# Performance work log

Measured on AMD Instinct MI355X. Metric: run time of the kernel, lower is better.

Reference implementation:

```python
import jax, jax.numpy as jnp
import numpy as np

NEG_SLOPE = 0.2
EPS = 1e-16
HEADS1, OUT1 = 4, 32
HEADS2, OUT2 = 1, 32


def _gat_conv(x, W, a_src, a_dst, bias, src, dst, num_nodes, heads, out_c, concat):
    # x: [N, F_in], W: [F_in, heads*out_c], a_*: [heads, out_c]
    h = (x @ W).reshape(num_nodes, heads, out_c)            # [N, H, C]
    alpha_src = (h * a_src).sum(-1)                          # [N, H]
    alpha_dst = (h * a_dst).sum(-1)                          # [N, H]
    e = jax.nn.leaky_relu(alpha_src[src] + alpha_dst[dst], NEG_SLOPE)  # [E, H]
    # softmax over incoming edges of each destination node (PyG softmax)
    m = jax.ops.segment_max(e, dst, num_segments=num_nodes)
    ex = jnp.exp(e - m[dst])
    s = jax.ops.segment_sum(ex, dst, num_segments=num_nodes)
    alpha = ex / (s[dst] + EPS)                              # [E, H]
    out = jax.ops.segment_sum(h[src] * alpha[:, :, None], dst,
                              num_segments=num_nodes)        # [N, H, C]
    out = out.reshape(num_nodes, heads * out_c) if concat else out.mean(axis=1)
    return out + bias


def setup_inputs() -> dict:
    key = jax.random.key(0)
    ks = jax.random.split(key, 10)
    N, E, F_IN = 50000, 1600000, 128
    sc = 0.1
    return {
        "x": jax.random.normal(ks[0], (N, F_IN), jnp.float32),
        "edge_index": jax.random.randint(ks[1], (2, E), 0, N, jnp.int32),
        "W1": jax.random.normal(ks[2], (F_IN, HEADS1 * OUT1), jnp.float32) * sc,
        "a_src1": jax.random.normal(ks[3], (HEADS1, OUT1), jnp.float32) * sc,
        "a_dst1": jax.random.normal(ks[4], (HEADS1, OUT1), jnp.float32) * sc,
        "b1": jax.random.normal(ks[5], (HEADS1 * OUT1,), jnp.float32) * sc,
        "W2": jax.random.normal(ks[6], (HEADS1 * OUT1, HEADS2 * OUT2), jnp.float32) * sc,
        "a_src2": jax.random.normal(ks[7], (HEADS2, OUT2), jnp.float32) * sc,
        "a_dst2": jax.random.normal(ks[8], (HEADS2, OUT2), jnp.float32) * sc,
        "b2": jax.random.normal(ks[9], (OUT2,), jnp.float32) * sc,
    }


def reference(x, edge_index, W1, a_src1, a_dst1, b1, W2, a_src2, a_dst2, b2):
    N = x.shape[0]
    # PyG GATConv default add_self_loops=True
    loops = jnp.arange(N, dtype=edge_index.dtype)
    src = jnp.concatenate([edge_index[0], loops])
    dst = jnp.concatenate([edge_index[1], loops])
    h = _gat_conv(x, W1, a_src1, a_dst1, b1, src, dst, N, HEADS1, OUT1, True)
    h = jax.nn.elu(h)
    return _gat_conv(h, W2, a_src2, a_dst2, b2, src, dst, N, HEADS2, OUT2, False)
```

## Files before the change

kernel.cpp:

```cpp
#include <hip/hip_runtime.h>
#include <math.h>

#define NEG_SLOPE 0.2f
#define EPSV 1e-16f
#define NPART 8

typedef _Float16 half4 __attribute__((ext_vector_type(4)));
typedef _Float16 half8 __attribute__((ext_vector_type(8)));
typedef float floatx2 __attribute__((ext_vector_type(2)));
typedef float f32x4 __attribute__((ext_vector_type(4)));


__global__ void k_scan_blk(const int* __restrict__ degp, int N,
                           int* __restrict__ rowptr, int* __restrict__ bsum){
    int b = blockIdx.x, t = threadIdx.x;
    int base = b * 1024 + t * 4;
    int v[4];
    #pragma unroll
    for (int j = 0; j < 4; j++){
        int n = base + j, s = 0;
        if (n < N){
            #pragma unroll
            for (int p = 0; p < NPART; p++) s += degp[p * N + n];
        }
        v[j] = s;
    }
    int s = v[0] + v[1] + v[2] + v[3];
    int lane = t & 63, wid = t >> 6;
    int x = s;
    #pragma unroll
    for (int off = 1; off < 64; off <<= 1){
        int y = __shfl_up(x, off, 64);
        if (lane >= off) x += y;
    }
    __shared__ int ws[4];
    if (lane == 63) ws[wid] = x;
    __syncthreads();
    int woff = 0;
    for (int w = 0; w < wid; w++) woff += ws[w];
    int run = woff + x - s;
    #pragma unroll
    for (int j = 0; j < 4; j++){
        if (base + j < N) rowptr[base + j] = run;
        run += v[j];
    }
    if (t == 255) bsum[b] = woff + x;
}

__global__ void k_finalize(const int* __restrict__ bsum, const int* __restrict__ degp,
                           int N, int ET,
                           int* __restrict__ rowptr, int* __restrict__ poff){
    int b = blockIdx.x, t = threadIdx.x;
    int n = b * 256 + t;
    int chunk = (b * 256) >> 10;
    int off = 0;
    for (int c = 0; c < chunk; c++) off += bsum[c];
    if (n < N){
        int r = rowptr[n] + off;
        rowptr[n] = r;
        int run = r;
        #pragma unroll
        for (int p = 0; p < NPART; p++){
            poff[p * N + n] = run;
            run += degp[p * N + n];
        }
    }
    if (n == 0) rowptr[N] = ET;
}

__launch_bounds__(256)
__global__ void k_scatter2(const int* __restrict__ ei, int E, int ET, int N,
                           const int* __restrict__ poff,
                           const unsigned short* __restrict__ rank,
                           int* __restrict__ csr_src){
    int i = blockIdx.x * 256 + threadIdx.x;
    if (i >= ET) return;
    int s, d;
    if (i < E){ s = ei[i]; d = ei[E + i]; } else { s = i - E; d = s; }
    int pr = rank[i];
    int p = pr >> 13, r = pr & 0x1FFF;
    csr_src[poff[p * N + d] + r] = s;
}


__launch_bounds__(256)
__global__ void k_hist(const int* __restrict__ ei, int E, int ET, int N,
                       unsigned int* __restrict__ degp, unsigned short* __restrict__ rank){
    int t = threadIdx.x;
    int p = __builtin_amdgcn_s_getreg((3 << 11) | 20) & 7;
    int base = blockIdx.x * 1024 + t;
    #pragma unroll
    for (int j = 0; j < 4; j++){
        int i = base + j * 256;
        if (i < ET){
            int d = (i < E) ? ei[E + i] : (i - E);
            unsigned r = __hip_atomic_fetch_add(&degp[(size_t)p * N + d], 1u,
                             __ATOMIC_RELAXED, __HIP_MEMORY_SCOPE_WORKGROUP);
            rank[i] = (unsigned short)((p << 13) | r);
        }
    }
}


__global__ void k_pack(const float* __restrict__ W1, const float* __restrict__ a_src,
                       const float* __restrict__ a_dst,
                       _Float16* __restrict__ W1f, _Float16* __restrict__ Uf){
    int b = blockIdx.x, t = threadIdx.x;
    if (b < 32){
        #pragma unroll
        for (int i = 0; i < 2; i++){
            int idx = t + 256 * i;
            int jj = idx & 7, ln = idx >> 3;
            int kt = b & 3, ct = b >> 2;
            int k = kt * 32 + (ln >> 4) * 8 + jj;
            int col = ct * 16 + (ln & 15);
            W1f[b * 512 + idx] = (_Float16)W1[k * 128 + col];
        }
        return;
    }
    __shared__ float U[128 * 8];
    if (t < 128){
        #pragma unroll
        for (int h = 0; h < 4; h++){
            float s = 0.f, d = 0.f;
            for (int cc = 0; cc < 32; cc++){
                float w = W1[t * 128 + h * 32 + cc];
                s += w * a_src[h * 32 + cc];
                d += w * a_dst[h * 32 + cc];
            }
            U[t * 8 + h]     = s;
            U[t * 8 + h + 4] = d;
        }
    }
    __syncthreads();
    for (int idx = t; idx < 4 * 64 * 8; idx += 256){
        int jj = idx & 7, ln = (idx >> 3) & 63, kt = idx >> 9;
        int k = kt * 32 + (ln >> 4) * 8 + jj;
        int col = ln & 15;
        Uf[idx] = (_Float16)(col < 8 ? U[k * 8 + col] : 0.f);
    }
}


__launch_bounds__(256)
__global__ void k_gemm1(const float* __restrict__ x, const _Float16* __restrict__ W1f,
                        const _Float16* __restrict__ Uf,
                        _Float16* __restrict__ h1h, float* __restrict__ asrc1,
                        float* __restrict__ adst1, int N){
    int t = threadIdx.x;
    int w = t >> 6, lane = t & 63;
    int arow = blockIdx.x * 64 + w * 16 + (lane & 15);
    bool arow_ok = (arow < N);
    const float4* xr = (const float4*)&x[(size_t)(arow_ok ? arow : 0) << 7];
    const half8* Wf = (const half8*)W1f;
    const half8* Uv = (const half8*)Uf;

    f32x4 acc[8];
    #pragma unroll
    for (int c = 0; c < 8; c++) acc[c] = (f32x4)0.f;
    f32x4 accA = (f32x4)0.f;

    #pragma unroll
    for (int kt = 0; kt < 4; kt++){
        half8 af;
        if (arow_ok){
            float4 p0 = xr[kt * 8 + (lane >> 4) * 2];
            float4 p1 = xr[kt * 8 + (lane >> 4) * 2 + 1];
            af[0] = (_Float16)p0.x; af[1] = (_Float16)p0.y;
            af[2] = (_Float16)p0.z; af[3] = (_Float16)p0.w;
            af[4] = (_Float16)p1.x; af[5] = (_Float16)p1.y;
            af[6] = (_Float16)p1.z; af[7] = (_Float16)p1.w;
        } else {
            af[0] = (_Float16)0.f; af[1] = (_Float16)0.f;
            af[2] = (_Float16)0.f; af[3] = (_Float16)0.f;
            af[4] = (_Float16)0.f; af[5] = (_Float16)0.f;
            af[6] = (_Float16)0.f; af[7] = (_Float16)0.f;
        }
        #pragma unroll
        for (int ct = 0; ct < 8; ct++){
            half8 bf = Wf[(ct * 4 + kt) * 64 + lane];
            acc[ct] = __builtin_amdgcn_mfma_f32_16x16x32_f16(af, bf, acc[ct], 0, 0, 0);
        }
        half8 uf = Uv[kt * 64 + lane];
        accA = __builtin_amdgcn_mfma_f32_16x16x32_f16(af, uf, accA, 0, 0, 0);
    }

    int g = lane >> 4, j = lane & 15;
    int rowbase = blockIdx.x * 64 + w * 16 + g * 4;
    #pragma unroll
    for (int r = 0; r < 4; r++){
        int n = rowbase + r;
        if (n >= N) continue;
        _Float16* hrow = &h1h[(size_t)n << 7];
        #pragma unroll
        for (int ct = 0; ct < 8; ct++)
            hrow[ct * 16 + j] = (_Float16)acc[ct][r];
        float av = accA[r];
        if (j < 4)            asrc1[n * 4 + j]       = av;
        else if (j < 8)       adst1[n * 4 + (j - 4)] = av;
    }
}


__launch_bounds__(256)
__global__ void k_agg1(const int* __restrict__ rowptr, const int* __restrict__ csr_src,
                       const float* __restrict__ asrc1, const float* __restrict__ adst1,
                       const _Float16* __restrict__ h1h,
                       const float* __restrict__ b1, float* __restrict__ x2, int N){
    int t = threadIdx.x;
    int lane = t & 63;
    int g = lane >> 4, l = lane & 15, head = l >> 2;
    int n = blockIdx.x * 16 + ((t >> 6) << 2) + g;
    bool valid = (n < N);
    int nn = valid ? n : 0;
    int start = rowptr[nn], end = rowptr[nn + 1];
    float adn = adst1[(nn << 2) + head];
    const char* hb = (const char*)h1h;
    const char* ab = (const char*)asrc1;
    int hoff = l << 4;
    int aoff = head << 2;
    floatx2 r0[4], r1[4], r2[4], r3[4];
    #pragma unroll
    for (int j = 0; j < 4; j++){
        r0[j] = (floatx2)0.f; r1[j] = (floatx2)0.f;
        r2[j] = (floatx2)0.f; r3[j] = (floatx2)0.f;
    }
    float s0a = 0.f, s1a = 0.f, s2a = 0.f, s3a = 0.f;
    int i = start;
    for (; i + 3 < end; i += 4){
        int sa = csr_src[i];
        int sb = csr_src[i + 1];
        int sc = csr_src[i + 2];
        int sd = csr_src[i + 3];
        float ea = *(const float*)(ab + (sa << 4) + aoff) + adn;
        float eb = *(const float*)(ab + (sb << 4) + aoff) + adn;
        float ec = *(const float*)(ab + (sc << 4) + aoff) + adn;
        float ed = *(const float*)(ab + (sd << 4) + aoff) + adn;
        ea = fmaxf(ea, NEG_SLOPE * ea);
        eb = fmaxf(eb, NEG_SLOPE * eb);
        ec = fmaxf(ec, NEG_SLOPE * ec);
        ed = fmaxf(ed, NEG_SLOPE * ed);
        float wa = __expf(ea);
        float wb = __expf(eb);
        float wc = __expf(ec);
        float wd = __expf(ed);
        half8 ha = *(const half8*)(hb + (sa << 8) + hoff);
        half8 hbv = *(const half8*)(hb + (sb << 8) + hoff);
        half8 hcv = *(const half8*)(hb + (sc << 8) + hoff);
        half8 hdv = *(const half8*)(hb + (sd << 8) + hoff);
        s0a += wa; s1a += wb; s2a += wc; s3a += wd;
        floatx2 wa2 = {wa, wa}, wb2 = {wb, wb}, wc2 = {wc, wc}, wd2 = {wd, wd};
        #pragma unroll
        for (int j = 0; j < 4; j++){
            floatx2 ca = {(float)ha[2*j], (float)ha[2*j+1]};
            floatx2 cb = {(float)hbv[2*j], (float)hbv[2*j+1]};
            floatx2 cc = {(float)hcv[2*j], (float)hcv[2*j+1]};
            floatx2 cd = {(float)hdv[2*j], (float)hdv[2*j+1]};
            r0[j] = wa2 * ca + r0[j];
            r1[j] = wb2 * cb + r1[j];
            r2[j] = wc2 * cc + r2[j];
            r3[j] = wd2 * cd + r3[j];
        }
    }
    for (; i < end; i++){
        int sa = csr_src[i];
        float ea = *(const float*)(ab + (sa << 4) + aoff) + adn;
        ea = fmaxf(ea, NEG_SLOPE * ea);
        float wa = __expf(ea);
        half8 ha = *(const half8*)(hb + (sa << 8) + hoff);
        s0a += wa;
        floatx2 wa2 = {wa, wa};
        #pragma unroll
        for (int j = 0; j < 4; j++){
            floatx2 ca = {(float)ha[2*j], (float)ha[2*j+1]};
            r0[j] = wa2 * ca + r0[j];
        }
    }
    if (valid){
        float ssum = (s0a + s1a) + (s2a + s3a);
        float inv = 1.f / (ssum + EPSV);
        float o[8];
        #pragma unroll
        for (int j = 0; j < 4; j++){
            floatx2 c = (r0[j] + r1[j]) + (r2[j] + r3[j]);
            float v0 = c.x * inv + b1[l * 8 + 2*j];
            float v1 = c.y * inv + b1[l * 8 + 2*j + 1];
            o[2*j]   = (v0 > 0.f) ? v0 : expm1f(v0);
            o[2*j+1] = (v1 > 0.f) ? v1 : expm1f(v1);
        }
        float4 o0 = {o[0], o[1], o[2], o[3]};
        float4 o1 = {o[4], o[5], o[6], o[7]};
        *(float4*)&x2[((size_t)n << 7) + (l << 3)]     = o0;
        *(float4*)&x2[((size_t)n << 7) + (l << 3) + 4] = o1;
    }
}


__launch_bounds__(256)
__global__ void k_gemm2(const float* __restrict__ x2, const float* __restrict__ W2,
                        const float* __restrict__ a_src, const float* __restrict__ a_dst,
                        _Float16* __restrict__ h2h, float* __restrict__ asrc2,
                        float* __restrict__ adst2, int N){
    __shared__ float Wl[128 * 32];
    __shared__ float xl[64 * 128];
    int t = threadIdx.x;
    int cg = t & 7, ns = t >> 3;
    for (int idx = t; idx < 1024; idx += 256)
        *(float4*)&Wl[idx * 4] = *(const float4*)&W2[idx * 4];
    int n0 = blockIdx.x * 64;
    for (int idx = t; idx < 2048; idx += 256){
        int row = idx >> 5, k4 = idx & 31;
        float4 v = {0.f, 0.f, 0.f, 0.f};
        if (n0 + row < N) v = *(const float4*)&x2[(size_t)(n0 + row) * 128 + k4 * 4];
        *(float4*)&xl[row * 128 + k4 * 4] = v;
    }
    __syncthreads();
    float4 acc0 = {0,0,0,0}, acc1 = {0,0,0,0};
    #pragma unroll 2
    for (int k = 0; k < 128; k += 4){
        float4 xv0 = *(float4*)&xl[(ns      ) * 128 + k];
        float4 xv1 = *(float4*)&xl[(ns + 32) * 128 + k];
        #pragma unroll
        for (int kk = 0; kk < 4; kk++){
            float4 w = *(float4*)&Wl[(k + kk) * 32 + cg * 4];
            float x0 = ((float*)&xv0)[kk];
            float x1 = ((float*)&xv1)[kk];
            acc0.x = fmaf(x0, w.x, acc0.x); acc0.y = fmaf(x0, w.y, acc0.y);
            acc0.z = fmaf(x0, w.z, acc0.z); acc0.w = fmaf(x0, w.w, acc0.w);
            acc1.x = fmaf(x1, w.x, acc1.x); acc1.y = fmaf(x1, w.y, acc1.y);
            acc1.z = fmaf(x1, w.z, acc1.z); acc1.w = fmaf(x1, w.w, acc1.w);
        }
    }
    float4 a4s = *(const float4*)&a_src[cg * 4];
    float4 a4d = *(const float4*)&a_dst[cg * 4];
    float4 accs[2] = {acc0, acc1};
    #pragma unroll
    for (int j = 0; j < 2; j++){
        int n = n0 + ns + 32 * j;
        if (n >= N) continue;
        float4 a = accs[j];
        half4 hv;
        hv.x = (_Float16)a.x; hv.y = (_Float16)a.y;
        hv.z = (_Float16)a.z; hv.w = (_Float16)a.w;
        *(half4*)&h2h[((size_t)n << 5) + (cg << 2)] = hv;
        float vs = a.x * a4s.x + a.y * a4s.y + a.z * a4s.z + a.w * a4s.w;
        float vd = a.x * a4d.x + a.y * a4d.y + a.z * a4d.z + a.w * a4d.w;
        #pragma unroll
        for (int m = 1; m <= 4; m <<= 1){
            vs += __shfl_xor(vs, m, 64);
            vd += __shfl_xor(vd, m, 64);
        }
        if (cg == 0){ asrc2[n] = vs; adst2[n] = vd; }
    }
}


__launch_bounds__(256)
__global__ void k_agg2(const int* __restrict__ rowptr, const int* __restrict__ csr_src,
                       const float* __restrict__ asrc2, const float* __restrict__ adst2,
                       const _Float16* __restrict__ h2h,
                       const float* __restrict__ b2, float* __restrict__ out, int N){
    int t = threadIdx.x;
    int lane = t & 63;
    int g = lane >> 3, l = lane & 7;
    int n = blockIdx.x * 32 + ((t >> 6) << 3) + g;
    bool valid = (n < N);
    int nn = valid ? n : 0;
    int start = rowptr[nn], end = rowptr[nn + 1];
    float adn = adst2[nn];
    const char* hb = (const char*)h2h;
    const char* ab = (const char*)asrc2;
    int hoff = l << 3;
    floatx2 a0[2], a1[2], a2[2], a3[2];
    a0[0] = (floatx2)0.f; a0[1] = (floatx2)0.f;
    a1[0] = (floatx2)0.f; a1[1] = (floatx2)0.f;
    a2[0] = (floatx2)0.f; a2[1] = (floatx2)0.f;
    a3[0] = (floatx2)0.f; a3[1] = (floatx2)0.f;
    float s0a = 0.f, s1a = 0.f, s2a = 0.f, s3a = 0.f;
    int i = start;
    for (; i + 3 < end; i += 4){
        int sa = csr_src[i];
        int sb = csr_src[i + 1];
        int sc = csr_src[i + 2];
        int sd = csr_src[i + 3];
        float ea = *(const float*)(ab + (sa << 2)) + adn;
        float eb = *(const float*)(ab + (sb << 2)) + adn;
        float ec = *(const float*)(ab + (sc << 2)) + adn;
        float ed = *(const float*)(ab + (sd << 2)) + adn;
        ea = fmaxf(ea, NEG_SLOPE * ea);
        eb = fmaxf(eb, NEG_SLOPE * eb);
        ec = fmaxf(ec, NEG_SLOPE * ec);
        ed = fmaxf(ed, NEG_SLOPE * ed);
        float wa = __expf(ea);
        float wb = __expf(eb);
        float wc = __expf(ec);
        float wd = __expf(ed);
        half4 ha = *(const half4*)(hb + (sa << 6) + hoff);
        half4 hbv = *(const half4*)(hb + (sb << 6) + hoff);
        half4 hcv = *(const half4*)(hb + (sc << 6) + hoff);
        half4 hdv = *(const half4*)(hb + (sd << 6) + hoff);
        s0a += wa; s1a += wb; s2a += wc; s3a += wd;
        floatx2 wa2 = {wa, wa}, wb2 = {wb, wb}, wc2 = {wc, wc}, wd2 = {wd, wd};
        floatx2 ca0 = {(float)ha.x, (float)ha.y},  ca1 = {(float)ha.z, (float)ha.w};
        floatx2 cb0 = {(float)hbv.x, (float)hbv.y}, cb1 = {(float)hbv.z, (float)hbv.w};
        floatx2 cc0 = {(float)hcv.x, (float)hcv.y}, cc1 = {(float)hcv.z, (float)hcv.w};
        floatx2 cd0 = {(float)hdv.x, (float)hdv.y}, cd1 = {(float)hdv.z, (float)hdv.w};
        a0[0] = wa2 * ca0 + a0[0]; a0[1] = wa2 * ca1 + a0[1];
        a1[0] = wb2 * cb0 + a1[0]; a1[1] = wb2 * cb1 + a1[1];
        a2[0] = wc2 * cc0 + a2[0]; a2[1] = wc2 * cc1 + a2[1];
        a3[0] = wd2 * cd0 + a3[0]; a3[1] = wd2 * cd1 + a3[1];
    }
    for (; i < end; i++){
        int sa = csr_src[i];
        float ea = *(const float*)(ab + (sa << 2)) + adn;
        ea = fmaxf(ea, NEG_SLOPE * ea);
        float wa = __expf(ea);
        half4 ha = *(const half4*)(hb + (sa << 6) + hoff);
        s0a += wa;
        floatx2 wa2 = {wa, wa};
        floatx2 ca0 = {(float)ha.x, (float)ha.y}, ca1 = {(float)ha.z, (float)ha.w};
        a0[0] = wa2 * ca0 + a0[0]; a0[1] = wa2 * ca1 + a0[1];
    }
    if (valid){
        floatx2 m0 = (a0[0] + a1[0]) + (a2[0] + a3[0]);
        floatx2 m1 = (a0[1] + a1[1]) + (a2[1] + a3[1]);
        float ssum = (s0a + s1a) + (s2a + s3a);
        float inv = 1.f / (ssum + EPSV);
        const float4 b4 = *(const float4*)&b2[l * 4];
        float4 o;
        o.x = m0.x * inv + b4.x; o.y = m0.y * inv + b4.y;
        o.z = m1.x * inv + b4.z; o.w = m1.y * inv + b4.w;
        *(float4*)&out[((size_t)n << 5) + (l << 2)] = o;
    }
}


extern "C" void kernel_launch(void* const* d_in, const int* in_sizes, int n_in,
                              void* d_out, int out_size, void* d_ws, size_t ws_size,
                              hipStream_t stream){
    const float* x      = (const float*)d_in[0];
    const int*   ei     = (const int*)  d_in[1];
    const float* W1     = (const float*)d_in[2];
    const float* a_src1 = (const float*)d_in[3];
    const float* a_dst1 = (const float*)d_in[4];
    const float* b1     = (const float*)d_in[5];
    const float* W2     = (const float*)d_in[6];
    const float* a_src2 = (const float*)d_in[7];
    const float* a_dst2 = (const float*)d_in[8];
    const float* b2     = (const float*)d_in[9];
    float* out = (float*)d_out;

    int N  = in_sizes[0] / 128;
    int E  = in_sizes[1] / 2;
    int ET = E + N;
    int nScanBlk = (N + 1023) / 1024;
    int G  = (ET + 255) / 256;
    int GH = (ET + 1023) / 1024;
    int nGemmBlk = (N + 63) / 64;

    char* ws = (char*)d_ws;
    size_t off = 0;
    auto alloc = [&](size_t bytes) -> char* {
        char* p = ws + off;
        off += (bytes + 255) & ~(size_t)255;
        return p;
    };
    int*            degp    = (int*)           alloc((size_t)NPART * N * 4);
    int*            rowptr  = (int*)           alloc((size_t)(N + 1) * 4);
    int*            bsum    = (int*)           alloc((size_t)nScanBlk * 4);
    unsigned short* rank    = (unsigned short*)alloc((size_t)ET * 2);
    int*            poff    = (int*)           alloc((size_t)NPART * N * 4);
    int*            csr_src = (int*)           alloc((size_t)ET * 4);
    _Float16*       h1h     = (_Float16*)      alloc((size_t)N * 128 * 2);
    float*          x2      = (float*)         alloc((size_t)N * 128 * 4);
    float*          asrc1   = (float*)         alloc((size_t)N * 4 * 4);
    float*          adst1   = (float*)         alloc((size_t)N * 4 * 4);
    _Float16*       h2h     = (_Float16*)      alloc((size_t)N * 32 * 2);
    float*          asrc2   = (float*)         alloc((size_t)N * 4);
    float*          adst2   = (float*)         alloc((size_t)N * 4);
    _Float16*       W1f     = (_Float16*)      alloc((size_t)32 * 512 * 2);
    _Float16*       Uf      = (_Float16*)      alloc((size_t)4 * 512 * 2);

    hipMemsetAsync(degp, 0, (size_t)NPART * N * 4, stream);
    hipLaunchKernelGGL(k_pack,   dim3(33), dim3(256), 0, stream, W1, a_src1, a_dst1, W1f, Uf);
    hipLaunchKernelGGL(k_hist,   dim3(GH), dim3(256), 0, stream, ei, E, ET, N, (unsigned int*)degp, rank);
    hipLaunchKernelGGL(k_gemm1,  dim3(nGemmBlk), dim3(256), 0, stream, x, W1f, Uf, h1h, asrc1, adst1, N);
    hipLaunchKernelGGL(k_scan_blk,  dim3(nScanBlk), dim3(256), 0, stream, degp, N, rowptr, bsum);
    hipLaunchKernelGGL(k_finalize,  dim3((N + 255) / 256), dim3(256), 0, stream, bsum, degp, N, ET, rowptr, poff);
    hipLaunchKernelGGL(k_scatter2,  dim3(G), dim3(256), 0, stream, ei, E, ET, N, poff, rank, csr_src);
    hipLaunchKernelGGL(k_agg1,      dim3((N + 15) / 16), dim3(256), 0, stream, rowptr, csr_src, asrc1, adst1, h1h, b1, x2, N);
    hipLaunchKernelGGL(k_gemm2,     dim3((N + 63) / 64), dim3(256), 0, stream, x2, W2, a_src2, a_dst2, h2h, asrc2, adst2, N);
    hipLaunchKernelGGL(k_agg2,      dim3((N + 31) / 32), dim3(256), 0, stream, rowptr, csr_src, asrc2, adst2, h2h, b2, out, N);
}
```

Measured before the change: 314.3 us.

## Precompute per-edge attention weights in CSR scatter and unroll layer-1 aggregation by eight

The CSR scatter kernel now also computes the leaky-ReLU and exp attention weight for all four heads of each edge. It writes them to a new per-edge float4 buffer in CSR order. The layer-1 aggregation reads these weights contiguously instead of gathering source attention scores and recomputing exp, and its main loop is unrolled from four to eight edges. This removes per-edge exp work and the random score gathers from aggregation, at the cost of an extra 16-byte scattered write and read per edge.

```diff
diff --git a/kernel.cpp b/kernel.cpp
--- a/kernel.cpp
+++ b/kernel.cpp
@@ -69,17 +69,30 @@
 }
 
 __launch_bounds__(256)
-__global__ void k_scatter2(const int* __restrict__ ei, int E, int ET, int N,
-                           const int* __restrict__ poff,
-                           const unsigned short* __restrict__ rank,
-                           int* __restrict__ csr_src){
+__global__ void k_scatter_w(const int* __restrict__ ei, int E, int ET, int N,
+                            const int* __restrict__ poff,
+                            const unsigned short* __restrict__ rank,
+                            const float* __restrict__ asrc1, const float* __restrict__ adst1,
+                            int* __restrict__ csr_src, float4* __restrict__ w4buf){
     int i = blockIdx.x * 256 + threadIdx.x;
     if (i >= ET) return;
     int s, d;
     if (i < E){ s = ei[i]; d = ei[E + i]; } else { s = i - E; d = s; }
     int pr = rank[i];
     int p = pr >> 13, r = pr & 0x1FFF;
-    csr_src[poff[p * N + d] + r] = s;
+    int pos = poff[p * N + d] + r;
+    csr_src[pos] = s;
+    float4 as = *(const float4*)&asrc1[s << 2];
+    float4 ad = *(const float4*)&adst1[d << 2];
+    float4 e = {as.x + ad.x, as.y + ad.y, as.z + ad.z, as.w + ad.w};
+    e.x = fmaxf(e.x, NEG_SLOPE * e.x);
+    e.y = fmaxf(e.y, NEG_SLOPE * e.y);
+    e.z = fmaxf(e.z, NEG_SLOPE * e.z);
+    e.w = fmaxf(e.w, NEG_SLOPE * e.w);
+    float4 w;
+    w.x = __expf(e.x); w.y = __expf(e.y);
+    w.z = __expf(e.z); w.w = __expf(e.w);
+    w4buf[pos] = w;
 }
 
 
@@ -204,7 +217,7 @@
 
 __launch_bounds__(256)
 __global__ void k_agg1(const int* __restrict__ rowptr, const int* __restrict__ csr_src,
-                       const float* __restrict__ asrc1, const float* __restrict__ adst1,
+                       const float* __restrict__ wbuf4,
                        const _Float16* __restrict__ h1h,
                        const float* __restrict__ b1, float* __restrict__ x2, int N){
     int t = threadIdx.x;
@@ -214,11 +227,10 @@
     bool valid = (n < N);
     int nn = valid ? n : 0;
     int start = rowptr[nn], end = rowptr[nn + 1];
-    float adn = adst1[(nn << 2) + head];
     const char* hb = (const char*)h1h;
-    const char* ab = (const char*)asrc1;
+    const char* wb = (const char*)wbuf4;
     int hoff = l << 4;
-    int aoff = head << 2;
+    int woff = head << 2;
     floatx2 r0[4], r1[4], r2[4], r3[4];
     #pragma unroll
     for (int j = 0; j < 4; j++){
@@ -227,47 +239,58 @@
     }
     float s0a = 0.f, s1a = 0.f, s2a = 0.f, s3a = 0.f;
     int i = start;
-    for (; i + 3 < end; i += 4){
+    for (; i + 7 < end; i += 8){
         int sa = csr_src[i];
         int sb = csr_src[i + 1];
         int sc = csr_src[i + 2];
         int sd = csr_src[i + 3];
-        float ea = *(const float*)(ab + (sa << 4) + aoff) + adn;
-        float eb = *(const float*)(ab + (sb << 4) + aoff) + adn;
-        float ec = *(const float*)(ab + (sc << 4) + aoff) + adn;
-        float ed = *(const float*)(ab + (sd << 4) + aoff) + adn;
-        ea = fmaxf(ea, NEG_SLOPE * ea);
-        eb = fmaxf(eb, NEG_SLOPE * eb);
-        ec = fmaxf(ec, NEG_SLOPE * ec);
-        ed = fmaxf(ed, NEG_SLOPE * ed);
-        float wa = __expf(ea);
-        float wb = __expf(eb);
-        float wc = __expf(ec);
-        float wd = __expf(ed);
-        half8 ha = *(const half8*)(hb + (sa << 8) + hoff);
-        half8 hbv = *(const half8*)(hb + (sb << 8) + hoff);
-        half8 hcv = *(const half8*)(hb + (sc << 8) + hoff);
-        half8 hdv = *(const half8*)(hb + (sd << 8) + hoff);
-        s0a += wa; s1a += wb; s2a += wc; s3a += wd;
-        floatx2 wa2 = {wa, wa}, wb2 = {wb, wb}, wc2 = {wc, wc}, wd2 = {wd, wd};
+        int se = csr_src[i + 4];
+        int sf = csr_src[i + 5];
+        int sg = csr_src[i + 6];
+        int sh = csr_src[i + 7];
+        float wa = *(const float*)(wb + ((size_t)(i    ) << 4) + woff);
+        float wbv= *(const float*)(wb + ((size_t)(i + 1) << 4) + woff);
+        float wc = *(const float*)(wb + ((size_t)(i + 2) << 4) + woff);
+        float wd = *(const float*)(wb + ((size_t)(i + 3) << 4) + woff);
+        float we = *(const float*)(wb + ((size_t)(i + 4) << 4) + woff);
+        float wf = *(const float*)(wb + ((size_t)(i + 5) << 4) + woff);
+        float wg = *(const float*)(wb + ((size_t)(i + 6) << 4) + woff);
+        float wh = *(const float*)(wb + ((size_t)(i + 7) << 4) + woff);
+        half8 ha = *(const half8*)(hb + ((size_t)sa << 8) + hoff);
+        half8 hbx= *(const half8*)(hb + ((size_t)sb << 8) + hoff);
+        half8 hc = *(const half8*)(hb + ((size_t)sc << 8) + hoff);
+        half8 hd = *(const half8*)(hb + ((size_t)sd << 8) + hoff);
+        half8 he = *(const half8*)(hb + ((size_t)se << 8) + hoff);
+        half8 hf = *(const half8*)(hb + ((size_t)sf << 8) + hoff);
+        half8 hg = *(const half8*)(hb + ((size_t)sg << 8) + hoff);
+        half8 hh = *(const half8*)(hb + ((size_t)sh << 8) + hoff);
+        s0a += wa + we; s1a += wbv + wf; s2a += wc + wg; s3a += wd + wh;
+        floatx2 wa2 = {wa, wa}, wb2 = {wbv, wbv}, wc2 = {wc, wc}, wd2 = {wd, wd};
+        floatx2 we2 = {we, we}, wf2 = {wf, wf}, wg2 = {wg, wg}, wh2 = {wh, wh};
         #pragma unroll
         for (int j = 0; j < 4; j++){
-            floatx2 ca = {(float)ha[2*j], (float)ha[2*j+1]};
-            floatx2 cb = {(float)hbv[2*j], (float)hbv[2*j+1]};
-            floatx2 cc = {(float)hcv[2*j], (float)hcv[2*j+1]};
-            floatx2 cd = {(float)hdv[2*j], (float)hdv[2*j+1]};
+            floatx2 ca = {(float)ha[2*j],  (float)ha[2*j+1]};
+            floatx2 cb = {(float)hbx[2*j], (float)hbx[2*j+1]};
+            floatx2 cc = {(float)hc[2*j],  (float)hc[2*j+1]};
+            floatx2 cd = {(float)hd[2*j],  (float)hd[2*j+1]};
+            floatx2 ce = {(float)he[2*j],  (float)he[2*j+1]};
+            floatx2 cf = {(float)hf[2*j],  (float)hf[2*j+1]};
+            floatx2 cg = {(float)hg[2*j],  (float)hg[2*j+1]};
+            floatx2 ch = {(float)hh[2*j],  (float)hh[2*j+1]};
             r0[j] = wa2 * ca + r0[j];
             r1[j] = wb2 * cb + r1[j];
             r2[j] = wc2 * cc + r2[j];
             r3[j] = wd2 * cd + r3[j];
+            r0[j] = we2 * ce + r0[j];
+            r1[j] = wf2 * cf + r1[j];
+            r2[j] = wg2 * cg + r2[j];
+            r3[j] = wh2 * ch + r3[j];
         }
     }
     for (; i < end; i++){
         int sa = csr_src[i];
-        float ea = *(const float*)(ab + (sa << 4) + aoff) + adn;
-        ea = fmaxf(ea, NEG_SLOPE * ea);
-        float wa = __expf(ea);
-        half8 ha = *(const half8*)(hb + (sa << 8) + hoff);
+        float wa = *(const float*)(wb + ((size_t)i << 4) + woff);
+        half8 ha = *(const half8*)(hb + ((size_t)sa << 8) + hoff);
         s0a += wa;
         floatx2 wa2 = {wa, wa};
         #pragma unroll
@@ -480,6 +503,7 @@
     float*          adst2   = (float*)         alloc((size_t)N * 4);
     _Float16*       W1f     = (_Float16*)      alloc((size_t)32 * 512 * 2);
     _Float16*       Uf      = (_Float16*)      alloc((size_t)4 * 512 * 2);
+    float4*         w4buf   = (float4*)        alloc((size_t)ET * 16);
 
     hipMemsetAsync(degp, 0, (size_t)NPART * N * 4, stream);
     hipLaunchKernelGGL(k_pack,   dim3(33), dim3(256), 0, stream, W1, a_src1, a_dst1, W1f, Uf);
@@ -487,8 +511,9 @@
     hipLaunchKernelGGL(k_gemm1,  dim3(nGemmBlk), dim3(256), 0, stream, x, W1f, Uf, h1h, asrc1, adst1, N);
     hipLaunchKernelGGL(k_scan_blk,  dim3(nScanBlk), dim3(256), 0, stream, degp, N, rowptr, bsum);
     hipLaunchKernelGGL(k_finalize,  dim3((N + 255) / 256), dim3(256), 0, stream, bsum, degp, N, ET, rowptr, poff);
-    hipLaunchKernelGGL(k_scatter2,  dim3(G), dim3(256), 0, stream, ei, E, ET, N, poff, rank, csr_src);
-    hipLaunchKernelGGL(k_agg1,      dim3((N + 15) / 16), dim3(256), 0, stream, rowptr, csr_src, asrc1, adst1, h1h, b1, x2, N);
+    hipLaunchKernelGGL(k_scatter_w, dim3(G), dim3(256), 0, stream, ei, E, ET, N, poff, rank,
+                       asrc1, adst1, csr_src, w4buf);
+    hipLaunchKernelGGL(k_agg1,      dim3((N + 15) / 16), dim3(256), 0, stream, rowptr, csr_src, (const float*)w4buf, h1h, b1, x2, N);
     hipLaunchKernelGGL(k_gemm2,     dim3((N + 63) / 64), dim3(256), 0, stream, x2, W2, a_src2, a_dst2, h2h, asrc2, adst2, N);
     hipLaunchKernelGGL(k_agg2,      dim3((N + 31) / 32), dim3(256), 0, stream, rowptr, csr_src, asrc2, adst2, h2h, b2, out, N);
 }
```

New measurement: 349.3 us. 11.1% more time.

## Build CSR with atomic cursors and unroll aggregation gathers by eight

Applied to the files above, without the earlier changes.

Replaces the rank-based CSR build, where the histogram recorded a per-edge rank and the scatter computed positions from it, with a cursor-based scatter. The histogram now only counts degrees, and the scatter claims its slot with an atomicAdd on a per-partition cursor, so the rank array is no longer written or read. The partition is chosen by block index instead of the hardware XCC id, and the atomics move from workgroup scope to device scope. Both aggregation kernels now issue eight neighbour gathers per iteration into scalar FMA accumulators instead of four packed-float2 accumulators, to raise memory-level parallelism. The cost is extra atomic traffic in the scatter, a non-deterministic neighbour order, and higher register pressure in the aggregation kernels.

```diff
diff --git a/kernel.cpp b/kernel.cpp
--- a/kernel.cpp
+++ b/kernel.cpp
@@ -7,7 +7,6 @@
 
 typedef _Float16 half4 __attribute__((ext_vector_type(4)));
 typedef _Float16 half8 __attribute__((ext_vector_type(8)));
-typedef float floatx2 __attribute__((ext_vector_type(2)));
 typedef float f32x4 __attribute__((ext_vector_type(4)));
 
 
@@ -49,7 +48,7 @@
 
 __global__ void k_finalize(const int* __restrict__ bsum, const int* __restrict__ degp,
                            int N, int ET,
-                           int* __restrict__ rowptr, int* __restrict__ poff){
+                           int* __restrict__ rowptr, int* __restrict__ cursor){
     int b = blockIdx.x, t = threadIdx.x;
     int n = b * 256 + t;
     int chunk = (b * 256) >> 10;
@@ -61,44 +60,41 @@
         int run = r;
         #pragma unroll
         for (int p = 0; p < NPART; p++){
-            poff[p * N + n] = run;
+            cursor[p * N + n] = run;
             run += degp[p * N + n];
         }
     }
     if (n == 0) rowptr[N] = ET;
 }
 
-__launch_bounds__(256)
-__global__ void k_scatter2(const int* __restrict__ ei, int E, int ET, int N,
-                           const int* __restrict__ poff,
-                           const unsigned short* __restrict__ rank,
-                           int* __restrict__ csr_src){
+
+__launch_bounds__(256)
+__global__ void k_hist(const int* __restrict__ ei, int E, int ET, int N,
+                       unsigned int* __restrict__ degp){
+    int t = threadIdx.x;
+    int p = blockIdx.x & (NPART - 1);
+    int base = blockIdx.x * 1024 + t;
+    #pragma unroll
+    for (int j = 0; j < 4; j++){
+        int i = base + j * 256;
+        if (i < ET){
+            int d = (i < E) ? ei[E + i] : (i - E);
+            atomicAdd(&degp[(size_t)p * N + d], 1u);
+        }
+    }
+}
+
+
+__launch_bounds__(256)
+__global__ void k_scatter_c(const int* __restrict__ ei, int E, int ET, int N,
+                            int* __restrict__ cursor, int* __restrict__ csr_src){
     int i = blockIdx.x * 256 + threadIdx.x;
     if (i >= ET) return;
     int s, d;
     if (i < E){ s = ei[i]; d = ei[E + i]; } else { s = i - E; d = s; }
-    int pr = rank[i];
-    int p = pr >> 13, r = pr & 0x1FFF;
-    csr_src[poff[p * N + d] + r] = s;
-}
-
-
-__launch_bounds__(256)
-__global__ void k_hist(const int* __restrict__ ei, int E, int ET, int N,
-                       unsigned int* __restrict__ degp, unsigned short* __restrict__ rank){
-    int t = threadIdx.x;
-    int p = __builtin_amdgcn_s_getreg((3 << 11) | 20) & 7;
-    int base = blockIdx.x * 1024 + t;
-    #pragma unroll
-    for (int j = 0; j < 4; j++){
-        int i = base + j * 256;
-        if (i < ET){
-            int d = (i < E) ? ei[E + i] : (i - E);
-            unsigned r = __hip_atomic_fetch_add(&degp[(size_t)p * N + d], 1u,
-                             __ATOMIC_RELAXED, __HIP_MEMORY_SCOPE_WORKGROUP);
-            rank[i] = (unsigned short)((p << 13) | r);
-        }
-    }
+    int p = (i >> 10) & (NPART - 1);
+    int pos = atomicAdd(&cursor[p * N + d], 1);
+    csr_src[pos] = s;
 }
 
 
@@ -219,74 +215,54 @@
     const char* ab = (const char*)asrc1;
     int hoff = l << 4;
     int aoff = head << 2;
-    floatx2 r0[4], r1[4], r2[4], r3[4];
-    #pragma unroll
-    for (int j = 0; j < 4; j++){
-        r0[j] = (floatx2)0.f; r1[j] = (floatx2)0.f;
-        r2[j] = (floatx2)0.f; r3[j] = (floatx2)0.f;
-    }
-    float s0a = 0.f, s1a = 0.f, s2a = 0.f, s3a = 0.f;
+    float acc[8];
+    #pragma unroll
+    for (int j = 0; j < 8; j++) acc[j] = 0.f;
+    float s0 = 0.f, s1 = 0.f, s2 = 0.f, s3 = 0.f;
     int i = start;
-    for (; i + 3 < end; i += 4){
-        int sa = csr_src[i];
-        int sb = csr_src[i + 1];
-        int sc = csr_src[i + 2];
-        int sd = csr_src[i + 3];
-        float ea = *(const float*)(ab + (sa << 4) + aoff) + adn;
-        float eb = *(const float*)(ab + (sb << 4) + aoff) + adn;
-        float ec = *(const float*)(ab + (sc << 4) + aoff) + adn;
-        float ed = *(const float*)(ab + (sd << 4) + aoff) + adn;
-        ea = fmaxf(ea, NEG_SLOPE * ea);
-        eb = fmaxf(eb, NEG_SLOPE * eb);
-        ec = fmaxf(ec, NEG_SLOPE * ec);
-        ed = fmaxf(ed, NEG_SLOPE * ed);
-        float wa = __expf(ea);
-        float wb = __expf(eb);
-        float wc = __expf(ec);
-        float wd = __expf(ed);
-        half8 ha = *(const half8*)(hb + (sa << 8) + hoff);
-        half8 hbv = *(const half8*)(hb + (sb << 8) + hoff);
-        half8 hcv = *(const half8*)(hb + (sc << 8) + hoff);
-        half8 hdv = *(const half8*)(hb + (sd << 8) + hoff);
-        s0a += wa; s1a += wb; s2a += wc; s3a += wd;
-        floatx2 wa2 = {wa, wa}, wb2 = {wb, wb}, wc2 = {wc, wc}, wd2 = {wd, wd};
-        #pragma unroll
-        for (int j = 0; j < 4; j++){
-            floatx2 ca = {(float)ha[2*j], (float)ha[2*j+1]};
-            floatx2 cb = {(float)hbv[2*j], (float)hbv[2*j+1]};
-            floatx2 cc = {(float)hcv[2*j], (float)hcv[2*j+1]};
-            floatx2 cd = {(float)hdv[2*j], (float)hdv[2*j+1]};
-            r0[j] = wa2 * ca + r0[j];
-            r1[j] = wb2 * cb + r1[j];
-            r2[j] = wc2 * cc + r2[j];
-            r3[j] = wd2 * cd + r3[j];
+    for (; i + 7 < end; i += 8){
+        int sv[8];
+        #pragma unroll
+        for (int q = 0; q < 8; q++) sv[q] = csr_src[i + q];
+        half8 hv[8];
+        #pragma unroll
+        for (int q = 0; q < 8; q++)
+            hv[q] = *(const half8*)(hb + ((size_t)sv[q] << 8) + hoff);
+        float wv[8];
+        #pragma unroll
+        for (int q = 0; q < 8; q++){
+            float e = *(const float*)(ab + ((size_t)sv[q] << 4) + aoff) + adn;
+            e = fmaxf(e, NEG_SLOPE * e);
+            wv[q] = __expf(e);
+        }
+        s0 += wv[0] + wv[4]; s1 += wv[1] + wv[5];
+        s2 += wv[2] + wv[6]; s3 += wv[3] + wv[7];
+        #pragma unroll
+        for (int q = 0; q < 8; q++){
+            #pragma unroll
+            for (int j = 0; j < 8; j++)
+                acc[j] = fmaf((float)hv[q][j], wv[q], acc[j]);
         }
     }
     for (; i < end; i++){
         int sa = csr_src[i];
-        float ea = *(const float*)(ab + (sa << 4) + aoff) + adn;
-        ea = fmaxf(ea, NEG_SLOPE * ea);
-        float wa = __expf(ea);
-        half8 ha = *(const half8*)(hb + (sa << 8) + hoff);
-        s0a += wa;
-        floatx2 wa2 = {wa, wa};
-        #pragma unroll
-        for (int j = 0; j < 4; j++){
-            floatx2 ca = {(float)ha[2*j], (float)ha[2*j+1]};
-            r0[j] = wa2 * ca + r0[j];
-        }
+        float e = *(const float*)(ab + ((size_t)sa << 4) + aoff) + adn;
+        e = fmaxf(e, NEG_SLOPE * e);
+        float wa = __expf(e);
+        half8 ha = *(const half8*)(hb + ((size_t)sa << 8) + hoff);
+        s0 += wa;
+        #pragma unroll
+        for (int j = 0; j < 8; j++)
+            acc[j] = fmaf((float)ha[j], wa, acc[j]);
     }
     if (valid){
-        float ssum = (s0a + s1a) + (s2a + s3a);
+        float ssum = (s0 + s1) + (s2 + s3);
         float inv = 1.f / (ssum + EPSV);
         float o[8];
         #pragma unroll
-        for (int j = 0; j < 4; j++){
-            floatx2 c = (r0[j] + r1[j]) + (r2[j] + r3[j]);
-            float v0 = c.x * inv + b1[l * 8 + 2*j];
-            float v1 = c.y * inv + b1[l * 8 + 2*j + 1];
-            o[2*j]   = (v0 > 0.f) ? v0 : expm1f(v0);
-            o[2*j+1] = (v1 > 0.f) ? v1 : expm1f(v1);
+        for (int j = 0; j < 8; j++){
+            float v = acc[j] * inv + b1[l * 8 + j];
+            o[j] = (v > 0.f) ? v : expm1f(v);
         }
         float4 o0 = {o[0], o[1], o[2], o[3]};
         float4 o1 = {o[4], o[5], o[6], o[7]};
@@ -371,65 +347,55 @@
     const char* hb = (const char*)h2h;
     const char* ab = (const char*)asrc2;
     int hoff = l << 3;
-    floatx2 a0[2], a1[2], a2[2], a3[2];
-    a0[0] = (floatx2)0.f; a0[1] = (floatx2)0.f;
-    a1[0] = (floatx2)0.f; a1[1] = (floatx2)0.f;
-    a2[0] = (floatx2)0.f; a2[1] = (floatx2)0.f;
-    a3[0] = (floatx2)0.f; a3[1] = (floatx2)0.f;
-    float s0a = 0.f, s1a = 0.f, s2a = 0.f, s3a = 0.f;
+    float acc[4];
+    #pragma unroll
+    for (int j = 0; j < 4; j++) acc[j] = 0.f;
+    float s0 = 0.f, s1 = 0.f, s2 = 0.f, s3 = 0.f;
     int i = start;
-    for (; i + 3 < end; i += 4){
-        int sa = csr_src[i];
-        int sb = csr_src[i + 1];
-        int sc = csr_src[i + 2];
-        int sd = csr_src[i + 3];
-        float ea = *(const float*)(ab + (sa << 2)) + adn;
-        float eb = *(const float*)(ab + (sb << 2)) + adn;
-        float ec = *(const float*)(ab + (sc << 2)) + adn;
-        float ed = *(const float*)(ab + (sd << 2)) + adn;
-        ea = fmaxf(ea, NEG_SLOPE * ea);
-        eb = fmaxf(eb, NEG_SLOPE * eb);
-        ec = fmaxf(ec, NEG_SLOPE * ec);
-        ed = fmaxf(ed, NEG_SLOPE * ed);
-        float wa = __expf(ea);
-        float wb = __expf(eb);
-        float wc = __expf(ec);
-        float wd = __expf(ed);
-        half4 ha = *(const half4*)(hb + (sa << 6) + hoff);
-        half4 hbv = *(const half4*)(hb + (sb << 6) + hoff);
-        half4 hcv = *(const half4*)(hb + (sc << 6) + hoff);
-        half4 hdv = *(const half4*)(hb + (sd << 6) + hoff);
-        s0a += wa; s1a += wb; s2a += wc; s3a += wd;
-        floatx2 wa2 = {wa, wa}, wb2 = {wb, wb}, wc2 = {wc, wc}, wd2 = {wd, wd};
-        floatx2 ca0 = {(float)ha.x, (float)ha.y},  ca1 = {(float)ha.z, (float)ha.w};
-        floatx2 cb0 = {(float)hbv.x, (float)hbv.y}, cb1 = {(float)hbv.z, (float)hbv.w};
-        floatx2 cc0 = {(float)hcv.x, (float)hcv.y}, cc1 = {(float)hcv.z, (float)hcv.w};
-        floatx2 cd0 = {(float)hdv.x, (float)hdv.y}, cd1 = {(float)hdv.z, (float)hdv.w};
-        a0[0] = wa2 * ca0 + a0[0]; a0[1] = wa2 * ca1 + a0[1];
-        a1[0] = wb2 * cb0 + a1[0]; a1[1] = wb2 * cb1 + a1[1];
-        a2[0] = wc2 * cc0 + a2[0]; a2[1] = wc2 * cc1 + a2[1];
-        a3[0] = wd2 * cd0 + a3[0]; a3[1] = wd2 * cd1 + a3[1];
+    for (; i + 7 < end; i += 8){
+        int sv[8];
+        #pragma unroll
+        for (int q = 0; q < 8; q++) sv[q] = csr_src[i + q];
+        half4 hv[8];
+        #pragma unroll
+        for (int q = 0; q < 8; q++)
+            hv[q] = *(const half4*)(hb + ((size_t)sv[q] << 6) + hoff);
+        float wv[8];
+        #pragma unroll
+        for (int q = 0; q < 8; q++){
+            float e = *(const float*)(ab + ((size_t)sv[q] << 2)) + adn;
+            e = fmaxf(e, NEG_SLOPE * e);
+            wv[q] = __expf(e);
+        }
+        s0 += wv[0] + wv[4]; s1 += wv[1] + wv[5];
+        s2 += wv[2] + wv[6]; s3 += wv[3] + wv[7];
+        #pragma unroll
+        for (int q = 0; q < 8; q++){
+            acc[0] = fmaf((float)hv[q].x, wv[q], acc[0]);
+            acc[1] = fmaf((float)hv[q].y, wv[q], acc[1]);
+            acc[2] = fmaf((float)hv[q].z, wv[q], acc[2]);
+            acc[3] = fmaf((float)hv[q].w, wv[q], acc[3]);
+        }
     }
     for (; i < end; i++){
         int sa = csr_src[i];
-        float ea = *(const float*)(ab + (sa << 2)) + adn;
-        ea = fmaxf(ea, NEG_SLOPE * ea);
-        float wa = __expf(ea);
-        half4 ha = *(const half4*)(hb + (sa << 6) + hoff);
-        s0a += wa;
-        floatx2 wa2 = {wa, wa};
-        floatx2 ca0 = {(float)ha.x, (float)ha.y}, ca1 = {(float)ha.z, (float)ha.w};
-        a0[0] = wa2 * ca0 + a0[0]; a0[1] = wa2 * ca1 + a0[1];
+        float e = *(const float*)(ab + ((size_t)sa << 2)) + adn;
+        e = fmaxf(e, NEG_SLOPE * e);
+        float wa = __expf(e);
+        half4 ha = *(const half4*)(hb + ((size_t)sa << 6) + hoff);
+        s0 += wa;
+        acc[0] = fmaf((float)ha.x, wa, acc[0]);
+        acc[1] = fmaf((float)ha.y, wa, acc[1]);
+        acc[2] = fmaf((float)ha.z, wa, acc[2]);
+        acc[3] = fmaf((float)ha.w, wa, acc[3]);
     }
     if (valid){
-        floatx2 m0 = (a0[0] + a1[0]) + (a2[0] + a3[0]);
-        floatx2 m1 = (a0[1] + a1[1]) + (a2[1] + a3[1]);
-        float ssum = (s0a + s1a) + (s2a + s3a);
+        float ssum = (s0 + s1) + (s2 + s3);
         float inv = 1.f / (ssum + EPSV);
         const float4 b4 = *(const float4*)&b2[l * 4];
         float4 o;
-        o.x = m0.x * inv + b4.x; o.y = m0.y * inv + b4.y;
-        o.z = m1.x * inv + b4.z; o.w = m1.y * inv + b4.w;
+        o.x = acc[0] * inv + b4.x; o.y = acc[1] * inv + b4.y;
+        o.z = acc[2] * inv + b4.z; o.w = acc[3] * inv + b4.w;
         *(float4*)&out[((size_t)n << 5) + (l << 2)] = o;
     }
 }
@@ -468,8 +434,7 @@
     int*            degp    = (int*)           alloc((size_t)NPART * N * 4);
     int*            rowptr  = (int*)           alloc((size_t)(N + 1) * 4);
     int*            bsum    = (int*)           alloc((size_t)nScanBlk * 4);
-    unsigned short* rank    = (unsigned short*)alloc((size_t)ET * 2);
-    int*            poff    = (int*)           alloc((size_t)NPART * N * 4);
+    int*            cursor  = (int*)           alloc((size_t)NPART * N * 4);
     int*            csr_src = (int*)           alloc((size_t)ET * 4);
     _Float16*       h1h     = (_Float16*)      alloc((size_t)N * 128 * 2);
     float*          x2      = (float*)         alloc((size_t)N * 128 * 4);
@@ -482,12 +447,12 @@
     _Float16*       Uf      = (_Float16*)      alloc((size_t)4 * 512 * 2);
 
     hipMemsetAsync(degp, 0, (size_t)NPART * N * 4, stream);
-    hipLaunchKernelGGL(k_pack,   dim3(33), dim3(256), 0, stream, W1, a_src1, a_dst1, W1f, Uf);
-    hipLaunchKernelGGL(k_hist,   dim3(GH), dim3(256), 0, stream, ei, E, ET, N, (unsigned int*)degp, rank);
-    hipLaunchKernelGGL(k_gemm1,  dim3(nGemmBlk), dim3(256), 0, stream, x, W1f, Uf, h1h, asrc1, adst1, N);
+    hipLaunchKernelGGL(k_pack,      dim3(33), dim3(256), 0, stream, W1, a_src1, a_dst1, W1f, Uf);
+    hipLaunchKernelGGL(k_hist,      dim3(GH), dim3(256), 0, stream, ei, E, ET, N, (unsigned int*)degp);
+    hipLaunchKernelGGL(k_gemm1,     dim3(nGemmBlk), dim3(256), 0, stream, x, W1f, Uf, h1h, asrc1, adst1, N);
     hipLaunchKernelGGL(k_scan_blk,  dim3(nScanBlk), dim3(256), 0, stream, degp, N, rowptr, bsum);
-    hipLaunchKernelGGL(k_finalize,  dim3((N + 255) / 256), dim3(256), 0, stream, bsum, degp, N, ET, rowptr, poff);
-    hipLaunchKernelGGL(k_scatter2,  dim3(G), dim3(256), 0, stream, ei, E, ET, N, poff, rank, csr_src);
+    hipLaunchKernelGGL(k_finalize,  dim3((N + 255) / 256), dim3(256), 0, stream, bsum, degp, N, ET, rowptr, cursor);
+    hipLaunchKernelGGL(k_scatter_c, dim3(G), dim3(256), 0, stream, ei, E, ET, N, cursor, csr_src);
     hipLaunchKernelGGL(k_agg1,      dim3((N + 15) / 16), dim3(256), 0, stream, rowptr, csr_src, asrc1, adst1, h1h, b1, x2, N);
     hipLaunchKernelGGL(k_gemm2,     dim3((N + 63) / 64), dim3(256), 0, stream, x2, W2, a_src2, a_dst2, h2h, asrc2, adst2, N);
     hipLaunchKernelGGL(k_agg2,      dim3((N + 31) / 32), dim3(256), 0, stream, rowptr, csr_src, asrc2, adst2, h2h, b2, out, N);
```

New measurement: 420.3 us. 1.34x slower.
